# Optimization experiments

Measured on AMD Instinct MI355X. Metric: run time of the kernel, lower is better.

The kernel has to match this reference:

```python
import jax, jax.numpy as jnp
import numpy as np

BL = 512  # sliding-window block length (init arg bl)


def setup_inputs() -> dict:
    key = jax.random.key(0)
    ks = jax.random.split(key, 8)
    L, qd, vd, c = 65536, 64, 64, 32  # c = q_dim // r1 = 32
    w = lambda k, sh: jax.random.normal(k, sh, jnp.float32) * 0.05
    return {
        "x1": jax.random.normal(ks[0], (1, qd, L), jnp.float32),
        "x2": jnp.zeros((1, vd, L), jnp.float32),
        "mask": jnp.ones((1, 1, L), jnp.float32),
        "Wq": w(ks[1], (c, qd)), "bq": jnp.zeros((c,), jnp.float32),
        "Wk": w(ks[2], (c, qd)), "bk": jnp.zeros((c,), jnp.float32),
        "Wv": w(ks[3], (c, vd)), "bv": jnp.zeros((c,), jnp.float32),
        "Wo": w(ks[4], (vd, c)), "bo": jnp.zeros((vd,), jnp.float32),
    }


def _sliding_att(x1, mask, Wq, bq, Wk, bk, Wv, bv, Wo, bo):
    bl = BL
    half = bl // 2
    W = bl + 2 * half
    B, _, L = x1.shape  # B == 1 (asserted in original)
    c = Wq.shape[0]
    vd = Wo.shape[0]

    # 1x1 conv1d projections == per-timestep matmul
    q = jnp.einsum('oc,bcl->bol', Wq, x1) + bq[None, :, None]
    k = jnp.einsum('oc,bcl->bol', Wk, x1) + bk[None, :, None]
    v = jnp.einsum('oc,bcl->bol', Wv, x1) + bv[None, :, None]

    nb = -(-L // bl)
    padL = nb * bl - L
    if padL:
        q = jnp.pad(q, ((0, 0), (0, 0), (0, padL)))
        k = jnp.pad(k, ((0, 0), (0, 0), (0, padL)))
        v = jnp.pad(v, ((0, 0), (0, 0), (0, padL)))
    base = jnp.pad(mask[:, 0:1, :], ((0, 0), (0, 0), (0, padL)))  # (1,1,nb*bl)

    # per-block queries: (nb, c, bl)
    qb = q[0].reshape(c, nb, bl).transpose(1, 0, 2)

    # pad K/V/mask by half on each side, gather overlapping windows (nb, c, W)
    kp = jnp.pad(k, ((0, 0), (0, 0), (half, half)))[0]
    vp = jnp.pad(v, ((0, 0), (0, 0), (half, half)))[0]
    bp = jnp.pad(base, ((0, 0), (0, 0), (half, half)))[0, 0]
    idx = jnp.arange(nb)[:, None] * bl + jnp.arange(W)[None, :]  # (nb, W)
    kw = kp[:, idx].transpose(1, 0, 2)  # (nb, c, W)
    vw = vp[:, idx].transpose(1, 0, 2)  # (nb, c, W)
    bw = bp[idx]                        # (nb, W)

    # causal window mask: query i attends to left half + up to i inside block
    rows = jnp.arange(bl)[:, None]
    cols = jnp.arange(W)[None, :]
    wmask = (cols <= half + rows).astype(jnp.float32)  # (bl, W)
    fmask = wmask[None, :, :] * bw[:, None, :]          # (nb, bl, W)

    # scalar dot attention with log-mask softmax trick (as in original)
    energy = jnp.einsum('ncq,nck->nqk', qb, kw) / jnp.sqrt(jnp.float32(c))
    att = jax.nn.softmax(energy + jnp.log(fmask + 1e-9), axis=-1) * fmask
    out = jnp.einsum('nck,nqk->ncq', vw, att)  # (nb, c, bl)

    out = jax.nn.relu(out)
    out = jnp.einsum('oc,ncl->nol', Wo, out) + bo[None, :, None]  # (nb, vd, bl)
    out = out.transpose(1, 0, 2).reshape(1, vd, nb * bl)[:, :, :L]
    return out * mask[:, 0:1, :]


def reference(x1, x2, mask, Wq, bq, Wk, bk, Wv, bv, Wo, bo):
    # stage == 'encoder': x2 is unused (value projected from x1)
    return _sliding_att(x1, mask, Wq, bq, Wk, bk, Wv, bv, Wo, bo)
```

## Files before the change

kernel.cpp:

```cpp
#include <hip/hip_runtime.h>
#include <hip/hip_bf16.h>
#include <math.h>

#define C    32
#define QD   64
#define VD   64
#define BLK  512
#define HALF 256

typedef __attribute__((ext_vector_type(8))) short bf16x8;
typedef __attribute__((ext_vector_type(4))) float f32x4;

static __device__ inline unsigned short f2bf(float x) {
    union { float f; unsigned u; } v; v.f = x;
    unsigned r = v.u + 0x7FFFu + ((v.u >> 16) & 1u);
    return (unsigned short)(r >> 16);
}

static __device__ inline unsigned pk2(float a, float b) {
    union { __hip_bfloat162 h; unsigned u; } x;
    x.h = __float22bfloat162_rn(make_float2(a, b));
    return x.u;
}

__global__ __launch_bounds__(256) void qkv_proj(
    const float* __restrict__ x1,
    const float* __restrict__ Wq, const float* __restrict__ bq,
    const float* __restrict__ Wk, const float* __restrict__ bk,
    const float* __restrict__ Wv, const float* __restrict__ bv,
    unsigned short* __restrict__ qT, unsigned short* __restrict__ kT,
    unsigned short* __restrict__ v2, int L)
{
    __shared__ uint4 lq[256], lk[256], lv[256];

    const int lane = threadIdx.x & 63;
    const int wv   = threadIdx.x >> 6;
    const int lo   = lane & 15;
    const int quad = lane >> 4;

    const int tile = blockIdx.x * 4 + wv;
    const int l    = tile * 16 + lo;
    const int ll   = wv * 16 + lo;

    float xv[16];
    #pragma unroll
    for (int kc = 0; kc < 2; ++kc)
        #pragma unroll
        for (int j = 0; j < 8; ++j)
            xv[kc * 8 + j] = x1[(size_t)(kc * 32 + quad * 8 + j) * L + l];

    bf16x8 B[2];
    #pragma unroll
    for (int kc = 0; kc < 2; ++kc) {
        union { unsigned u[4]; bf16x8 v; } bb;
        #pragma unroll
        for (int p = 0; p < 4; ++p)
            bb.u[p] = pk2(xv[kc * 8 + 2 * p], xv[kc * 8 + 2 * p + 1]);
        B[kc] = bb.v;
    }

    bf16x8 A[3][2][2];
    #pragma unroll
    for (int kind = 0; kind < 3; ++kind) {
        const float* __restrict__ Wp = (kind == 0) ? Wq : ((kind == 1) ? Wk : Wv);
        const float sc = (kind == 0) ? 0.17677669529663689f : 1.0f;
        #pragma unroll
        for (int ot = 0; ot < 2; ++ot) {
            #pragma unroll
            for (int kc = 0; kc < 2; ++kc) {
                const float* wp = Wp + (size_t)(ot * 16 + lo) * QD + kc * 32 + quad * 8;
                const float4 w0 = *(const float4*)wp;
                const float4 w1 = *(const float4*)(wp + 4);
                union { unsigned u[4]; bf16x8 v; } t;
                t.u[0] = pk2(w0.x * sc, w0.y * sc);
                t.u[1] = pk2(w0.z * sc, w0.w * sc);
                t.u[2] = pk2(w1.x * sc, w1.y * sc);
                t.u[3] = pk2(w1.z * sc, w1.w * sc);
                A[kind][ot][kc] = t.v;
            }
        }
    }

    const f32x4 zero = {0.f, 0.f, 0.f, 0.f};
    f32x4 acc[3][2];
    #pragma unroll
    for (int kind = 0; kind < 3; ++kind)
        #pragma unroll
        for (int ot = 0; ot < 2; ++ot) {
            f32x4 a = __builtin_amdgcn_mfma_f32_16x16x32_bf16(A[kind][ot][0], B[0], zero, 0, 0, 0);
            acc[kind][ot] = __builtin_amdgcn_mfma_f32_16x16x32_bf16(A[kind][ot][1], B[1], a, 0, 0, 0);
        }

    #pragma unroll
    for (int kind = 0; kind < 2; ++kind) {
        const float* __restrict__ bp = (kind == 0) ? bq : bk;
        const float sc = (kind == 0) ? 0.17677669529663689f : 1.0f;
        unsigned* __restrict__ ld = (unsigned*)((kind == 0) ? lq : lk);
        #pragma unroll
        for (int ot = 0; ot < 2; ++ot) {
            const float4 b4 = *(const float4*)(bp + ot * 16 + quad * 4);
            const float r0 = acc[kind][ot][0] + b4.x * sc;
            const float r1 = acc[kind][ot][1] + b4.y * sc;
            const float r2 = acc[kind][ot][2] + b4.z * sc;
            const float r3 = acc[kind][ot][3] + b4.w * sc;
            ld[ll * 16 + ot * 8 + quad * 2 + 0] = pk2(r0, r1);
            ld[ll * 16 + ot * 8 + quad * 2 + 1] = pk2(r2, r3);
        }
    }
    {
        unsigned short* __restrict__ lvs = (unsigned short*)lv;
        const int vb = ((ll >> 5) << 10) + ((ll & 31) - 0);
        #pragma unroll
        for (int ot = 0; ot < 2; ++ot) {
            const float4 b4 = *(const float4*)(bv + ot * 16 + quad * 4);
            const float* bp4 = (const float*)&b4;
            #pragma unroll
            for (int r = 0; r < 4; ++r)
                lvs[vb + (ot * 16 + quad * 4 + r) * 32] = f2bf(acc[2][ot][r] + bp4[r]);
        }
    }

    __syncthreads();

    const int t = threadIdx.x;
    const size_t blk16 = (size_t)blockIdx.x * 256;
    ((uint4*)qT)[blk16 + t] = lq[t];
    ((uint4*)kT)[blk16 + t] = lk[t];
    ((uint4*)v2)[blk16 + t] = lv[t];
}

__global__ __launch_bounds__(128, 4) void att_kernel(
    const unsigned short* __restrict__ qT,
    const unsigned short* __restrict__ kT,
    const unsigned short* __restrict__ v2,
    const float* __restrict__ mask,
    const float* __restrict__ Wo, const float* __restrict__ bo,
    float* __restrict__ out, int L)
{
    __shared__ float mrg[64 * 9];

    const int tid  = threadIdx.x;
    const int lane = tid & 63;
    const int h    = tid >> 6;
    const int lo   = lane & 15;
    const int quad = lane >> 4;

    const int id = blockIdx.x;
    const int w  = id & 127;
    const int s  = 31 - (id >> 7);
    const int wq0 = w * BLK + s * 16;

    const int kstart = max(0, w * BLK - HALF);
    const int n      = ((wq0 + 15 - kstart) >> 6) + 1;
    const int myq    = wq0 + lo;

    const bf16x8 qB = *(const bf16x8*)(qT + (size_t)myq * C + quad * 8);

    const f32x4 zero = {0.f, 0.f, 0.f, 0.f};
    f32x4 O0 = zero, O1 = zero;
    float psum = 0.f;

    const int qsl = lo + 16 * ((quad & 1) << 1);

    for (int j = h; j < n - 1; j += 2) {
        const int kb = kstart + (j << 6);

        f32x4 S[4];
        float4 fm4[4];
        const unsigned short* kp = kT + (size_t)(kb + lo) * C + quad * 8;
        #pragma unroll
        for (int t = 0; t < 4; ++t) {
            const bf16x8 kA = *(const bf16x8*)(kp + (size_t)(t * 16) * C);
            S[t] = __builtin_amdgcn_mfma_f32_16x16x32_bf16(kA, qB, zero, 0, 0, 0);
            fm4[t] = *(const float4*)(mask + kb + t * 16 + quad * 4);
        }

        unsigned wp[4][2];
        #pragma unroll
        for (int t = 0; t < 4; ++t) {
            const float* fmp = (const float*)&fm4[t];
            float p[4];
            #pragma unroll
            for (int r = 0; r < 4; ++r) {
                const float pd = __expf(S[t][r]) * (fmp[r] + 1e-9f);
                psum += pd;
                p[r] = pd * fmp[r];
            }
            wp[t][0] = pk2(p[0], p[1]);
            wp[t][1] = pk2(p[2], p[3]);
        }

        const unsigned short* vbase = v2 + ((size_t)(kb >> 6) << 11);
        #pragma unroll
        for (int g = 0; g < 2; ++g) {
            union { int i[4]; bf16x8 v; } pb;
            #pragma unroll
            for (int i = 0; i < 4; ++i) {
                const int src = qsl + 16 * (i >> 1);
                const int v0 = __shfl((int)wp[2 * g][i & 1], src);
                const int v1 = __shfl((int)wp[2 * g + 1][i & 1], src);
                pb.i[i] = (quad < 2) ? v0 : v1;
            }
            const bf16x8 vA0 = *(const bf16x8*)(vbase + g * 1024 + lo * 32 + quad * 8);
            const bf16x8 vA1 = *(const bf16x8*)(vbase + g * 1024 + (16 + lo) * 32 + quad * 8);
            O0 = __builtin_amdgcn_mfma_f32_16x16x32_bf16(vA0, pb.v, O0, 0, 0, 0);
            O1 = __builtin_amdgcn_mfma_f32_16x16x32_bf16(vA1, pb.v, O1, 0, 0, 0);
        }
    }

    if (((n - 1) & 1) == h) {
        const int kb = kstart + ((n - 1) << 6);

        f32x4 S[4];
        float4 fm4[4];
        const unsigned short* kp = kT + (size_t)(kb + lo) * C + quad * 8;
        #pragma unroll
        for (int t = 0; t < 4; ++t) {
            const bf16x8 kA = *(const bf16x8*)(kp + (size_t)(t * 16) * C);
            S[t] = __builtin_amdgcn_mfma_f32_16x16x32_bf16(kA, qB, zero, 0, 0, 0);
            fm4[t] = *(const float4*)(mask + kb + t * 16 + quad * 4);
        }

        unsigned wp[4][2];
        #pragma unroll
        for (int t = 0; t < 4; ++t) {
            const float* fmp = (const float*)&fm4[t];
            float p[4];
            #pragma unroll
            for (int r = 0; r < 4; ++r) {
                const int key = kb + t * 16 + quad * 4 + r;
                const float pd = (key <= myq) ? __expf(S[t][r]) * (fmp[r] + 1e-9f) : 0.f;
                psum += pd;
                p[r] = pd * fmp[r];
            }
            wp[t][0] = pk2(p[0], p[1]);
            wp[t][1] = pk2(p[2], p[3]);
        }

        const unsigned short* vbase = v2 + ((size_t)(kb >> 6) << 11);
        #pragma unroll
        for (int g = 0; g < 2; ++g) {
            union { int i[4]; bf16x8 v; } pb;
            #pragma unroll
            for (int i = 0; i < 4; ++i) {
                const int src = qsl + 16 * (i >> 1);
                const int v0 = __shfl((int)wp[2 * g][i & 1], src);
                const int v1 = __shfl((int)wp[2 * g + 1][i & 1], src);
                pb.i[i] = (quad < 2) ? v0 : v1;
            }
            const bf16x8 vA0 = *(const bf16x8*)(vbase + g * 1024 + lo * 32 + quad * 8);
            const bf16x8 vA1 = *(const bf16x8*)(vbase + g * 1024 + (16 + lo) * 32 + quad * 8);
            O0 = __builtin_amdgcn_mfma_f32_16x16x32_bf16(vA0, pb.v, O0, 0, 0, 0);
            O1 = __builtin_amdgcn_mfma_f32_16x16x32_bf16(vA1, pb.v, O1, 0, 0, 0);
        }
    }

    if (h == 1) {
        #pragma unroll
        for (int r = 0; r < 4; ++r) {
            mrg[lane * 9 + r]     = O0[r];
            mrg[lane * 9 + 4 + r] = O1[r];
        }
        mrg[lane * 9 + 8] = psum;
    }
    __syncthreads();
    if (h == 1) return;

    #pragma unroll
    for (int r = 0; r < 4; ++r) {
        O0[r] += mrg[lane * 9 + r];
        O1[r] += mrg[lane * 9 + 4 + r];
    }
    psum += mrg[lane * 9 + 8];

    float dsum = psum;
    dsum += __shfl_xor(dsum, 16);
    dsum += __shfl_xor(dsum, 32);
    const float inv = 1.f / dsum;

    unsigned tw[2][2];
    tw[0][0] = pk2(fmaxf(O0[0] * inv, 0.f), fmaxf(O0[1] * inv, 0.f));
    tw[0][1] = pk2(fmaxf(O0[2] * inv, 0.f), fmaxf(O0[3] * inv, 0.f));
    tw[1][0] = pk2(fmaxf(O1[0] * inv, 0.f), fmaxf(O1[1] * inv, 0.f));
    tw[1][1] = pk2(fmaxf(O1[2] * inv, 0.f), fmaxf(O1[3] * inv, 0.f));

    union { int i[4]; bf16x8 v; } tb;
    #pragma unroll
    for (int i = 0; i < 4; ++i) {
        const int src = qsl + 16 * (i >> 1);
        const int v0 = __shfl((int)tw[0][i & 1], src);
        const int v1 = __shfl((int)tw[1][i & 1], src);
        tb.i[i] = (quad < 2) ? v0 : v1;
    }

    const float mk = mask[myq];
    #pragma unroll
    for (int t = 0; t < 4; ++t) {
        float wtmp[8];
        *(float4*)&wtmp[0] = *(const float4*)(Wo + (size_t)(t * 16 + lo) * C + quad * 8);
        *(float4*)&wtmp[4] = *(const float4*)(Wo + (size_t)(t * 16 + lo) * C + quad * 8 + 4);
        union { unsigned u[4]; bf16x8 v; } wo;
        #pragma unroll
        for (int i = 0; i < 4; ++i) wo.u[i] = pk2(wtmp[2 * i], wtmp[2 * i + 1]);
        const f32x4 R = __builtin_amdgcn_mfma_f32_16x16x32_bf16(wo.v, tb.v, zero, 0, 0, 0);
        const float4 bo4 = *(const float4*)(bo + t * 16 + quad * 4);
        const float* bop = (const float*)&bo4;
        #pragma unroll
        for (int r = 0; r < 4; ++r)
            out[(size_t)(t * 16 + quad * 4 + r) * L + myq] = (R[r] + bop[r]) * mk;
    }
}

extern "C" void kernel_launch(void* const* d_in, const int* in_sizes, int n_in,
                              void* d_out, int out_size, void* d_ws, size_t ws_size,
                              hipStream_t stream)
{
    const float* x1   = (const float*)d_in[0];
    const float* mask = (const float*)d_in[2];
    const float* Wq   = (const float*)d_in[3];
    const float* bq   = (const float*)d_in[4];
    const float* Wk   = (const float*)d_in[5];
    const float* bk   = (const float*)d_in[6];
    const float* Wv   = (const float*)d_in[7];
    const float* bv   = (const float*)d_in[8];
    const float* Wo   = (const float*)d_in[9];
    const float* bo   = (const float*)d_in[10];
    float* out = (float*)d_out;

    const int L = in_sizes[0] / QD;
    unsigned short* qT = (unsigned short*)d_ws;
    unsigned short* kT = qT + (size_t)L * C;
    unsigned short* v2 = kT + (size_t)L * C;

    hipLaunchKernelGGL(qkv_proj, dim3(L / 64), dim3(256), 0, stream,
                       x1, Wq, bq, Wk, bk, Wv, bv, qT, kT, v2, L);

    hipLaunchKernelGGL(att_kernel, dim3(L / 16), dim3(128), 0, stream,
                       qT, kT, v2, mask, Wo, bo, out, L);
}
```

Before: 131.0 us.

## Share K/V tiles across four query waves via double-buffered LDS

The attention kernel now runs 256-thread blocks in which each of four waves handles a different 16-query strip of the same block. K and V chunks of 64 keys are loaded once per block into XOR-swizzled, double-buffered shared memory and prefetched one chunk ahead. This replaces the old two-wave split-key scheme and its LDS merge step. Each block now reads K/V from global memory once instead of once per 16-query strip. In exchange, it adds a block-wide barrier per chunk, and waves with fewer key chunks sit idle while the longest wave finishes.

```diff
diff --git a/kernel.cpp b/kernel.cpp
--- a/kernel.cpp
+++ b/kernel.cpp
@@ -109,7 +109,7 @@
     }
     {
         unsigned short* __restrict__ lvs = (unsigned short*)lv;
-        const int vb = ((ll >> 5) << 10) + ((ll & 31) - 0);
+        const int vb = ((ll >> 5) << 10) + (ll & 31);
         #pragma unroll
         for (int ot = 0; ot < 2; ++ot) {
             const float4 b4 = *(const float4*)(bv + ot * 16 + quad * 4);
@@ -129,7 +129,7 @@
     ((uint4*)v2)[blk16 + t] = lv[t];
 }
 
-__global__ __launch_bounds__(128, 4) void att_kernel(
+__global__ __launch_bounds__(256, 4) void att_kernel(
     const unsigned short* __restrict__ qT,
     const unsigned short* __restrict__ kT,
     const unsigned short* __restrict__ v2,
@@ -137,22 +137,25 @@
     const float* __restrict__ Wo, const float* __restrict__ bo,
     float* __restrict__ out, int L)
 {
-    __shared__ float mrg[64 * 9];
+    __shared__ unsigned short sK[2][2048];
+    __shared__ unsigned short sV[2][2048];
 
     const int tid  = threadIdx.x;
     const int lane = tid & 63;
-    const int h    = tid >> 6;
+    const int wv   = tid >> 6;
     const int lo   = lane & 15;
     const int quad = lane >> 4;
 
-    const int id = blockIdx.x;
-    const int w  = id & 127;
-    const int s  = 31 - (id >> 7);
+    const int id  = blockIdx.x;
+    const int w   = id & 127;
+    const int sub = 7 - (id >> 7);
+    const int s   = sub * 4 + wv;
     const int wq0 = w * BLK + s * 16;
 
     const int kstart = max(0, w * BLK - HALF);
-    const int n      = ((wq0 + 15 - kstart) >> 6) + 1;
-    const int myq    = wq0 + lo;
+    const int nwv  = ((wq0 + 15 - kstart) >> 6) + 1;
+    const int nmax = ((w * BLK + (sub * 4 + 3) * 16 + 15 - kstart) >> 6) + 1;
+    const int myq  = wq0 + lo;
 
     const bf16x8 qB = *(const bf16x8*)(qT + (size_t)myq * C + quad * 8);
 
@@ -162,116 +165,96 @@
 
     const int qsl = lo + 16 * ((quad & 1) << 1);
 
-    for (int j = h; j < n - 1; j += 2) {
-        const int kb = kstart + (j << 6);
-
-        f32x4 S[4];
-        float4 fm4[4];
-        const unsigned short* kp = kT + (size_t)(kb + lo) * C + quad * 8;
-        #pragma unroll
-        for (int t = 0; t < 4; ++t) {
-            const bf16x8 kA = *(const bf16x8*)(kp + (size_t)(t * 16) * C);
-            S[t] = __builtin_amdgcn_mfma_f32_16x16x32_bf16(kA, qB, zero, 0, 0, 0);
-            fm4[t] = *(const float4*)(mask + kb + t * 16 + quad * 4);
-        }
-
-        unsigned wp[4][2];
-        #pragma unroll
-        for (int t = 0; t < 4; ++t) {
-            const float* fmp = (const float*)&fm4[t];
-            float p[4];
+    const int wrOff = (tid * 16) ^ (((tid >> 3) & 3) << 4);
+    const int rdX   = (quad << 4) ^ (((lo >> 1) & 3) << 4);
+
+    {
+        const uint4 gk = ((const uint4*)(kT + (size_t)kstart * C))[tid];
+        const uint4 gv = ((const uint4*)(v2 + ((size_t)(kstart >> 6) << 11)))[tid];
+        *(uint4*)((char*)sK[0] + wrOff) = gk;
+        *(uint4*)((char*)sV[0] + wrOff) = gv;
+    }
+    __syncthreads();
+
+    for (int j = 0; j < nmax; ++j) {
+        const int kb  = kstart + (j << 6);
+        const int cur = j & 1;
+        const bool more = (j + 1) < nmax;
+
+        uint4 gk, gv;
+        if (more) {
+            const int kb1 = kb + 64;
+            gk = ((const uint4*)(kT + (size_t)kb1 * C))[tid];
+            gv = ((const uint4*)(v2 + ((size_t)(kb1 >> 6) << 11)))[tid];
+        }
+
+        if (j < nwv) {
+            f32x4 S[4];
+            float4 fm4[4];
+            const char* kbuf = (const char*)sK[cur];
             #pragma unroll
-            for (int r = 0; r < 4; ++r) {
-                const float pd = __expf(S[t][r]) * (fmp[r] + 1e-9f);
-                psum += pd;
-                p[r] = pd * fmp[r];
+            for (int t = 0; t < 4; ++t) {
+                const bf16x8 kA = *(const bf16x8*)(kbuf + ((t * 16 + lo) * 64 + rdX));
+                S[t] = __builtin_amdgcn_mfma_f32_16x16x32_bf16(kA, qB, zero, 0, 0, 0);
+                fm4[t] = *(const float4*)(mask + kb + t * 16 + quad * 4);
             }
-            wp[t][0] = pk2(p[0], p[1]);
-            wp[t][1] = pk2(p[2], p[3]);
-        }
-
-        const unsigned short* vbase = v2 + ((size_t)(kb >> 6) << 11);
-        #pragma unroll
-        for (int g = 0; g < 2; ++g) {
-            union { int i[4]; bf16x8 v; } pb;
+
+            unsigned wp[4][2];
+            if (j == nwv - 1) {
+                #pragma unroll
+                for (int t = 0; t < 4; ++t) {
+                    const float* fmp = (const float*)&fm4[t];
+                    float p[4];
+                    #pragma unroll
+                    for (int r = 0; r < 4; ++r) {
+                        const int key = kb + t * 16 + quad * 4 + r;
+                        const float pd = (key <= myq) ? __expf(S[t][r]) * (fmp[r] + 1e-9f) : 0.f;
+                        psum += pd;
+                        p[r] = pd * fmp[r];
+                    }
+                    wp[t][0] = pk2(p[0], p[1]);
+                    wp[t][1] = pk2(p[2], p[3]);
+                }
+            } else {
+                #pragma unroll
+                for (int t = 0; t < 4; ++t) {
+                    const float* fmp = (const float*)&fm4[t];
+                    float p[4];
+                    #pragma unroll
+                    for (int r = 0; r < 4; ++r) {
+                        const float pd = __expf(S[t][r]) * (fmp[r] + 1e-9f);
+                        psum += pd;
+                        p[r] = pd * fmp[r];
+                    }
+                    wp[t][0] = pk2(p[0], p[1]);
+                    wp[t][1] = pk2(p[2], p[3]);
+                }
+            }
+
+            const char* vbuf = (const char*)sV[cur];
             #pragma unroll
-            for (int i = 0; i < 4; ++i) {
-                const int src = qsl + 16 * (i >> 1);
-                const int v0 = __shfl((int)wp[2 * g][i & 1], src);
-                const int v1 = __shfl((int)wp[2 * g + 1][i & 1], src);
-                pb.i[i] = (quad < 2) ? v0 : v1;
+            for (int g = 0; g < 2; ++g) {
+                union { int i[4]; bf16x8 v; } pb;
+                #pragma unroll
+                for (int i = 0; i < 4; ++i) {
+                    const int src = qsl + 16 * (i >> 1);
+                    const int v0 = __shfl((int)wp[2 * g][i & 1], src);
+                    const int v1 = __shfl((int)wp[2 * g + 1][i & 1], src);
+                    pb.i[i] = (quad < 2) ? v0 : v1;
+                }
+                const bf16x8 vA0 = *(const bf16x8*)(vbuf + (g * 2048 + lo * 64 + rdX));
+                const bf16x8 vA1 = *(const bf16x8*)(vbuf + (g * 2048 + (16 + lo) * 64 + rdX));
+                O0 = __builtin_amdgcn_mfma_f32_16x16x32_bf16(vA0, pb.v, O0, 0, 0, 0);
+                O1 = __builtin_amdgcn_mfma_f32_16x16x32_bf16(vA1, pb.v, O1, 0, 0, 0);
             }
-            const bf16x8 vA0 = *(const bf16x8*)(vbase + g * 1024 + lo * 32 + quad * 8);
-            const bf16x8 vA1 = *(const bf16x8*)(vbase + g * 1024 + (16 + lo) * 32 + quad * 8);
-            O0 = __builtin_amdgcn_mfma_f32_16x16x32_bf16(vA0, pb.v, O0, 0, 0, 0);
-            O1 = __builtin_amdgcn_mfma_f32_16x16x32_bf16(vA1, pb.v, O1, 0, 0, 0);
-        }
-    }
-
-    if (((n - 1) & 1) == h) {
-        const int kb = kstart + ((n - 1) << 6);
-
-        f32x4 S[4];
-        float4 fm4[4];
-        const unsigned short* kp = kT + (size_t)(kb + lo) * C + quad * 8;
-        #pragma unroll
-        for (int t = 0; t < 4; ++t) {
-            const bf16x8 kA = *(const bf16x8*)(kp + (size_t)(t * 16) * C);
-            S[t] = __builtin_amdgcn_mfma_f32_16x16x32_bf16(kA, qB, zero, 0, 0, 0);
-            fm4[t] = *(const float4*)(mask + kb + t * 16 + quad * 4);
-        }
-
-        unsigned wp[4][2];
-        #pragma unroll
-        for (int t = 0; t < 4; ++t) {
-            const float* fmp = (const float*)&fm4[t];
-            float p[4];
-            #pragma unroll
-            for (int r = 0; r < 4; ++r) {
-                const int key = kb + t * 16 + quad * 4 + r;
-                const float pd = (key <= myq) ? __expf(S[t][r]) * (fmp[r] + 1e-9f) : 0.f;
-                psum += pd;
-                p[r] = pd * fmp[r];
-            }
-            wp[t][0] = pk2(p[0], p[1]);
-            wp[t][1] = pk2(p[2], p[3]);
-        }
-
-        const unsigned short* vbase = v2 + ((size_t)(kb >> 6) << 11);
-        #pragma unroll
-        for (int g = 0; g < 2; ++g) {
-            union { int i[4]; bf16x8 v; } pb;
-            #pragma unroll
-            for (int i = 0; i < 4; ++i) {
-                const int src = qsl + 16 * (i >> 1);
-                const int v0 = __shfl((int)wp[2 * g][i & 1], src);
-                const int v1 = __shfl((int)wp[2 * g + 1][i & 1], src);
-                pb.i[i] = (quad < 2) ? v0 : v1;
-            }
-            const bf16x8 vA0 = *(const bf16x8*)(vbase + g * 1024 + lo * 32 + quad * 8);
-            const bf16x8 vA1 = *(const bf16x8*)(vbase + g * 1024 + (16 + lo) * 32 + quad * 8);
-            O0 = __builtin_amdgcn_mfma_f32_16x16x32_bf16(vA0, pb.v, O0, 0, 0, 0);
-            O1 = __builtin_amdgcn_mfma_f32_16x16x32_bf16(vA1, pb.v, O1, 0, 0, 0);
-        }
-    }
-
-    if (h == 1) {
-        #pragma unroll
-        for (int r = 0; r < 4; ++r) {
-            mrg[lane * 9 + r]     = O0[r];
-            mrg[lane * 9 + 4 + r] = O1[r];
-        }
-        mrg[lane * 9 + 8] = psum;
-    }
-    __syncthreads();
-    if (h == 1) return;
-
-    #pragma unroll
-    for (int r = 0; r < 4; ++r) {
-        O0[r] += mrg[lane * 9 + r];
-        O1[r] += mrg[lane * 9 + 4 + r];
-    }
-    psum += mrg[lane * 9 + 8];
+        }
+
+        if (more) {
+            *(uint4*)((char*)sK[cur ^ 1] + wrOff) = gk;
+            *(uint4*)((char*)sV[cur ^ 1] + wrOff) = gv;
+        }
+        __syncthreads();
+    }
 
     float dsum = psum;
     dsum += __shfl_xor(dsum, 16);
@@ -335,6 +318,6 @@
     hipLaunchKernelGGL(qkv_proj, dim3(L / 64), dim3(256), 0, stream,
                        x1, Wq, bq, Wk, bk, Wv, bv, qT, kT, v2, L);
 
-    hipLaunchKernelGGL(att_kernel, dim3(L / 16), dim3(128), 0, stream,
+    hipLaunchKernelGGL(att_kernel, dim3(L / 64), dim3(256), 0, stream,
                        qT, kT, v2, mask, Wo, bo, out, L);
 }
```

Result: faster. 123.9 us (-5.4%).
